# Performance work log

Measured on AMD Instinct MI355X. Metric: run time of the kernel, lower is better.

## Reference

```python
import jax, jax.numpy as jnp
import numpy as np

B, P, C, H, W = 256, 512, 512, 7, 8
T = H * W  # 56
EPS = 1e-8


def setup_inputs() -> dict:
    key = jax.random.key(0)
    k1, k2, k3 = jax.random.split(key, 3)
    inp = jax.random.normal(k1, (B, C, H, W), dtype=jnp.float32)
    # xavier-uniform-like init for prototype (fan over last two dims as torch does)
    bound_p = float(np.sqrt(6.0 / (P + C * T)))
    prototype = jax.random.uniform(k2, (P, C, T), dtype=jnp.float32, minval=-bound_p, maxval=bound_p)
    bound_w = float(np.sqrt(6.0 / (C + 1)))
    fc_w = jax.random.uniform(k3, (1, C), dtype=jnp.float32, minval=-bound_w, maxval=bound_w)
    fc_b = jnp.zeros((1,), dtype=jnp.float32)
    return {"input": inp, "prototype": prototype, "fc_w": fc_w, "fc_b": fc_b}


def reference(input, prototype, fc_w, fc_b):
    # flatten spatial dims: (B, C, T)
    x = input.reshape(input.shape[0], input.shape[1], -1)
    # per-position cosine similarity over channel dim
    dots = jnp.einsum('bct,pct->bpt', x, prototype)          # (B, P, T)
    xn = jnp.linalg.norm(x, axis=1)                           # (B, T)
    pn = jnp.linalg.norm(prototype, axis=1)                   # (P, T)
    sim = dots / jnp.maximum(xn[:, None, :] * pn[None, :, :], EPS)
    att = jax.nn.softmax(sim, axis=-1)                        # (B, P, T)
    # attention-pooled elementwise product: (B, P, C)
    feat = jnp.einsum('bpt,bct,pct->bpc', att, x, prototype)
    # fc: Linear(C, 1) then relu, view to (B, P)
    out = jax.nn.relu(jnp.einsum('bpc,oc->bpo', feat, fc_w) + fc_b)
    return out.reshape(out.shape[0], out.shape[1])
```

## Files before the change

### kernel.cpp

```cpp
#include <hip/hip_runtime.h>
#include <hip/hip_bf16.h>
#include <math.h>

constexpr int kB = 256, kC = 512, kT = 56, kP = 512;
constexpr int kCT = kC * kT;

typedef short v4s __attribute__((ext_vector_type(4)));
typedef short v8s __attribute__((ext_vector_type(8)));
typedef float v4f __attribute__((ext_vector_type(4)));
typedef float v16f __attribute__((ext_vector_type(16)));

__device__ __forceinline__ unsigned pack_bf16(float a, float b) {
  __hip_bfloat16 ha = __float2bfloat16(a);
  __hip_bfloat16 hb = __float2bfloat16(b);
  unsigned short ua, ub;
  __builtin_memcpy(&ua, &ha, 2);
  __builtin_memcpy(&ub, &hb, 2);
  return (unsigned)ua | ((unsigned)ub << 16);
}

__device__ __forceinline__ v4s frag2(unsigned w0, unsigned w1) {
  unsigned u[2] = {w0, w1};
  v4s s;
  __builtin_memcpy(&s, u, 8);
  return s;
}

__device__ __forceinline__ v8s frag8(uint4 u) {
  v8s s;
  __builtin_memcpy(&s, &u, 16);
  return s;
}

#define GLOAD(gp, lp)                                                        \
  __builtin_amdgcn_global_load_lds(                                          \
      (const __attribute__((address_space(1))) unsigned*)(const unsigned*)(gp), \
      (__attribute__((address_space(3))) unsigned*)(unsigned*)(lp), 16, 0, 0)

__global__ __launch_bounds__(512) void prep_kernel(
    const float* __restrict__ x, const float* __restrict__ proto,
    const float* __restrict__ fcw,
    unsigned* __restrict__ xt, unsigned* __restrict__ xwt,
    unsigned* __restrict__ pt,
    float* __restrict__ xn2, float* __restrict__ pn2) {
  __shared__ float tile[128 * 57];
  __shared__ float fws[512];
  __shared__ float part[8][64];

  const int tid = threadIdx.x;
  const int bidx = blockIdx.x;
  const int n = bidx >> 2;
  const int ch = bidx & 3;
  const bool isx = (n < kB);
  const int row = isx ? n : (n - kB);
  const float* src = (isx ? x : proto) + (size_t)row * kCT;

  fws[tid] = fcw[tid & 511];

  const int g = tid >> 6, tt = tid & 63;

  const float* csrc = src + ch * (128 * 56);
#pragma unroll
  for (int it = 0; it < 4; ++it) {
    const int idx = it * 512 + tid;
    if (idx < 1792) {
      const int f0 = idx * 4;
      float4 v = *(const float4*)(csrc + f0);
      int c = (int)(((unsigned)f0 * 74899u) >> 22);
      int t = f0 - c * 56;
      tile[c * 57 + t] = v.x;
      tile[c * 57 + t + 1] = v.y;
      tile[c * 57 + t + 2] = v.z;
      tile[c * 57 + t + 3] = v.w;
    }
  }
  __syncthreads();

  float nacc = 0.f;
  if (tt < 56) {
#pragma unroll
    for (int cc2 = 0; cc2 < 16; ++cc2) {
      float u = tile[(g * 16 + cc2) * 57 + tt];
      nacc = fmaf(u, u, nacc);
    }
  }

#pragma unroll
  for (int it = 0; it < 7; ++it) {
    const int id = it * 512 + tid;
    const int t = id >> 6;
    const int cw = id & 63;
    float g0 = tile[(2 * cw) * 57 + t];
    float g1 = tile[(2 * cw + 1) * 57 + t];
    unsigned wd = pack_bf16(g0, g1);
    if (isx) {
      const size_t o = ((size_t)(t * kB + row)) * 256 + ch * 64 + cw;
      const int c = ch * 128 + 2 * cw;
      xt[o] = wd;
      xwt[o] = pack_bf16(g0 * fws[c], g1 * fws[c + 1]);
    } else {
      pt[((size_t)(t * kP + row)) * 256 + ch * 64 + cw] = wd;
    }
  }

  part[g][tt] = nacc;
  __syncthreads();
  if (tid < 56) {
    float s = 0.f;
#pragma unroll
    for (int gg = 0; gg < 8; ++gg) s += part[gg][tid];
    if (isx) atomicAdd(&xn2[row * 56 + tid], s);
    else     atomicAdd(&pn2[row * 56 + tid], s);
  }
}

constexpr int TILE = 64 * 32;
constexpr int BUF = 3 * TILE;

__global__ __launch_bounds__(256, 2) void proto_gemm_kernel(
    const unsigned* __restrict__ xt, const unsigned* __restrict__ xwt,
    const unsigned* __restrict__ pt,
    const float* __restrict__ xn2, const float* __restrict__ pn2,
    float* __restrict__ part) {
  __shared__ __align__(16) unsigned lds[3 * BUF];
  __shared__ float xnL[4 * 64], pnL[4 * 64];

  const int tid = threadIdx.x;
  const int l = tid & 63;
  const int w4 = tid >> 6;
  const int wm = w4 >> 1;
  const int wn = w4 & 1;

  int bid = (int)blockIdx.x;
  bid = (bid & 7) * 56 + (bid >> 3);
  const int b0 = (bid & 3) * 64;
  const int p0 = ((bid >> 2) & 7) * 64;
  const int tg = bid >> 5;

  {
    const int tl = tid >> 6, r = tid & 63;
    xnL[tid] = sqrtf(xn2[(b0 + r) * 56 + tg * 4 + tl]);
    pnL[tid] = sqrtf(pn2[(p0 + r) * 56 + tg * 4 + tl]);
  }
  __syncthreads();

  const int lrow = l >> 3, lch = l & 7;
  size_t xsrc[2], psrc[2];
  int ldst[2];
#pragma unroll
  for (int j = 0; j < 2; ++j) {
    const int row = w4 * 16 + j * 8 + lrow;
    const int ch4 = ((lch ^ (row & 7))) * 4;
    xsrc[j] = (size_t)(b0 + row) * 256 + ch4;
    psrc[j] = (size_t)(p0 + row) * 256 + ch4;
    ldst[j] = (w4 * 16 + j * 8) * 32;
  }

  const int fr = l & 31;
  const int hi = l >> 5;
  const int axb = (wm * 32 + fr) * 32;
  const int pxb = (wn * 32 + fr) * 32;
  const int frs = fr & 7;

  v16f aD, aW, sac, nac;
#pragma unroll
  for (int i = 0; i < 16; ++i) { aD[i] = 0.f; aW[i] = 0.f; sac[i] = 0.f; nac[i] = 0.f; }

  auto STAGE = [&](int s, int buf) {
    const int t = tg * 4 + (s >> 3);
    const size_t xo = (size_t)t * (kB * 256) + (size_t)((s & 7) * 32);
    const size_t po = (size_t)t * (kP * 256) + (size_t)((s & 7) * 32);
    unsigned* lb = lds + buf * BUF;
#pragma unroll
    for (int j = 0; j < 2; ++j) {
      GLOAD(xt + xsrc[j] + xo, lb + ldst[j]);
      GLOAD(xwt + xsrc[j] + xo, lb + TILE + ldst[j]);
      GLOAD(pt + psrc[j] + po, lb + 2 * TILE + ldst[j]);
    }
  };

  auto COMPUTE = [&](int s, int buf) {
    const unsigned* bx = lds + buf * BUF;
#pragma unroll
    for (int ks = 0; ks < 4; ++ks) {
      const int col = (((ks << 1) | hi) ^ frs) << 2;
      v8s xf = frag8(*(const uint4*)(bx + axb + col));
      v8s wf = frag8(*(const uint4*)(bx + TILE + axb + col));
      v8s pf = frag8(*(const uint4*)(bx + 2 * TILE + pxb + col));
      aD = __builtin_amdgcn_mfma_f32_32x32x16_bf16(xf, pf, aD, 0, 0, 0);
      aW = __builtin_amdgcn_mfma_f32_32x32x16_bf16(wf, pf, aW, 0, 0, 0);
    }
    if ((s & 7) == 7) {
      const int tl = s >> 3;
      const float pnv = pnL[tl * 64 + wn * 32 + fr];
#pragma unroll
      for (int i = 0; i < 16; ++i) {
        const int drow = (i & 3) + 8 * (i >> 2) + 4 * hi;
        const float xnv = xnL[tl * 64 + wm * 32 + drow];
        float den = fmaxf(xnv * pnv, 1e-8f);
        float sim = aD[i] * __builtin_amdgcn_rcpf(den);
        float e = __expf(sim);
        sac[i] += e;
        nac[i] = fmaf(e, aW[i], nac[i]);
        aD[i] = 0.f;
        aW[i] = 0.f;
      }
    }
  };

  STAGE(0, 0);
  STAGE(1, 1);

  int c0 = 0, c1 = 1, c2 = 2;
#pragma unroll 1
  for (int s = 0; s < 32; ++s) {
    if (s < 31) asm volatile("s_waitcnt vmcnt(6)" ::: "memory");
    else        asm volatile("s_waitcnt vmcnt(0)" ::: "memory");
    __builtin_amdgcn_s_barrier();
    __builtin_amdgcn_sched_barrier(0);
    COMPUTE(s, c0);
    if (s < 30) STAGE(s + 2, c2);
    const int tmp = c0; c0 = c1; c1 = c2; c2 = tmp;
  }

  float* psb = part + ((size_t)tg * 2 + 0) * 131072;
  float* pnb = part + ((size_t)tg * 2 + 1) * 131072;
#pragma unroll
  for (int i = 0; i < 16; ++i) {
    const int drow = (i & 3) + 8 * (i >> 2) + 4 * hi;
    const size_t o = (size_t)(b0 + wm * 32 + drow) * 512 + p0 + wn * 32 + fr;
    psb[o] = sac[i];
    pnb[o] = nac[i];
  }
}

__global__ __launch_bounds__(256) void merge_kernel(
    const float* __restrict__ part, const float* __restrict__ fcb,
    float* __restrict__ out) {
  const int pair = blockIdx.x * 256 + threadIdx.x;
  float S = 0.f, N = 0.f;
#pragma unroll
  for (int k = 0; k < 14; ++k) {
    S += part[((size_t)k * 2 + 0) * 131072 + pair];
    N += part[((size_t)k * 2 + 1) * 131072 + pair];
  }
  float o = N * __builtin_amdgcn_rcpf(S) + fcb[0];
  out[pair] = fmaxf(o, 0.f);
}

__global__ __launch_bounds__(1024) void proto_mfma_kernel(
    const float* __restrict__ x, const float* __restrict__ proto,
    const float* __restrict__ fcw, const float* __restrict__ fcb,
    float* __restrict__ out) {
  __shared__ unsigned xs[56 * 289];
  __shared__ unsigned ps[56 * 145];
  __shared__ unsigned pws[56 * 145];

  const int tid = threadIdx.x;
  const int l = tid & 63;
  const int w = tid >> 6;
  const int bq = w & 1;
  const int tq = w >> 1;
  const int t0 = tq * 7;

  const int n = blockIdx.y * 32 + blockIdx.x;
  const int p0 = (n >> 3) * 16;
  const int b0 = (n & 7) * 32;

  const bool act = (l < 56);
  const int lt = l;

  const int xbase0 = ((b0 + 2 * w + 0) * kC) * kT + lt;
  const int xbase1 = ((b0 + 2 * w + 1) * kC) * kT + lt;
  const int pbase = ((p0 + w) * kC) * kT + lt;

  const int arow = l & 15;
  const int q2 = (l >> 4) << 1;
  const int xoff = (bq * 16 + arow) * 9 + q2;
  const int poff = arow * 9 + q2;

  v4f acc[7][2];
#pragma unroll
  for (int ti = 0; ti < 7; ++ti) {
    acc[ti][0] = v4f{0.f, 0.f, 0.f, 0.f};
    acc[ti][1] = v4f{0.f, 0.f, 0.f, 0.f};
  }
  float xn2a = 0.f, xn2b = 0.f, pn2 = 0.f;

#pragma unroll 1
  for (int st = 0; st < 32; ++st) {
    const int k0 = st * 16;
    if (act) {
#pragma unroll
      for (int r = 0; r < 16; ++r) {
        const int cw = r & 7;
        const int c = k0 + 2 * cw;
        const int ga = ((r >> 3) ? xbase1 : xbase0) + c * kT;
        float g0 = x[ga], g1 = x[ga + kT];
        if (r >> 3) xn2b = fmaf(g0, g0, fmaf(g1, g1, xn2b));
        else xn2a = fmaf(g0, g0, fmaf(g1, g1, xn2a));
        xs[lt * 289 + (2 * w + (r >> 3)) * 9 + cw] = pack_bf16(g0, g1);
      }
#pragma unroll
      for (int cw = 0; cw < 8; ++cw) {
        const int c = k0 + 2 * cw;
        const int ga = pbase + c * kT;
        float g0 = proto[ga], g1 = proto[ga + kT];
        pn2 = fmaf(g0, g0, fmaf(g1, g1, pn2));
        ps[lt * 145 + w * 9 + cw] = pack_bf16(g0, g1);
        float f0 = fcw[c], f1 = fcw[c + 1];
        pws[lt * 145 + w * 9 + cw] = pack_bf16(g0 * f0, g1 * f1);
      }
    }
    __syncthreads();
#pragma unroll
    for (int ti = 0; ti < 7; ++ti) {
      const int t = t0 + ti;
      unsigned xw0 = xs[t * 289 + xoff];
      unsigned xw1 = xs[t * 289 + xoff + 1];
      unsigned pw0 = ps[t * 145 + poff];
      unsigned pw1 = ps[t * 145 + poff + 1];
      unsigned ww0 = pws[t * 145 + poff];
      unsigned ww1 = pws[t * 145 + poff + 1];
      v4s af = frag2(xw0, xw1);
      v4s bf = frag2(pw0, pw1);
      v4s wf = frag2(ww0, ww1);
      acc[ti][0] = __builtin_amdgcn_mfma_f32_16x16x16bf16_1k(af, bf, acc[ti][0], 0, 0, 0);
      acc[ti][1] = __builtin_amdgcn_mfma_f32_16x16x16bf16_1k(af, wf, acc[ti][1], 0, 0, 0);
    }
    __syncthreads();
  }

  float* xnorm = (float*)ps;
  float* pnorm = xnorm + 32 * 56;
  if (act) {
    xnorm[(2 * w + 0) * 56 + lt] = xn2a;
    xnorm[(2 * w + 1) * 56 + lt] = xn2b;
    pnorm[w * 56 + lt] = pn2;
  }
  __syncthreads();

  float* fm = (float*)xs;
  float* fsum = fm + 4096;
  float* fnum = fsum + 4096;
  const int pc = arow;
  const int qq = l >> 4;
#pragma unroll
  for (int i = 0; i < 4; ++i) {
    const int bl = bq * 16 + 4 * qq + i;
    float m = -3.0e38f;
    float sims[7];
#pragma unroll
    for (int ti = 0; ti < 7; ++ti) {
      const int t = t0 + ti;
      float den = fmaxf(sqrtf(xnorm[bl * 56 + t]) * sqrtf(pnorm[pc * 56 + t]), 1e-8f);
      float s = acc[ti][0][i] / den;
      sims[ti] = s;
      m = fmaxf(m, s);
    }
    float se = 0.f, nu = 0.f;
#pragma unroll
    for (int ti = 0; ti < 7; ++ti) {
      float e = __expf(sims[ti] - m);
      se += e;
      nu = fmaf(e, acc[ti][1][i], nu);
    }
    const int pair = bl * 16 + pc;
    fm[tq * 512 + pair] = m;
    fsum[tq * 512 + pair] = se;
    fnum[tq * 512 + pair] = nu;
  }
  __syncthreads();

  if (tid < 512) {
    float M = -3.0e38f;
#pragma unroll
    for (int k = 0; k < 8; ++k) M = fmaxf(M, fm[k * 512 + tid]);
    float S = 0.f, N = 0.f;
#pragma unroll
    for (int k = 0; k < 8; ++k) {
      float sc = __expf(fm[k * 512 + tid] - M);
      S = fmaf(fsum[k * 512 + tid], sc, S);
      N = fmaf(fnum[k * 512 + tid], sc, N);
    }
    float o = N / S + fcb[0];
    out[(b0 + (tid >> 4)) * kP + p0 + (tid & 15)] = fmaxf(o, 0.f);
  }
}

extern "C" void kernel_launch(void* const* d_in, const int* in_sizes, int n_in,
                              void* d_out, int out_size, void* d_ws, size_t ws_size,
                              hipStream_t stream) {
  const float* x = (const float*)d_in[0];
  const float* proto = (const float*)d_in[1];
  const float* fcw = (const float*)d_in[2];
  const float* fcb = (const float*)d_in[3];
  float* out = (float*)d_out;

  const size_t need = 73572352;
  if (ws_size >= need) {
    unsigned* xt = (unsigned*)d_ws;
    unsigned* xwt = xt + 3670016;
    unsigned* ptb = xt + 7340032;
    float* partb = (float*)(xt + 14680064);
    float* xn2b = (float*)(xt + 18350080);
    float* pn2b = xn2b + 14336;

    hipMemsetAsync(xn2b, 0, (14336 + 28672) * sizeof(float), stream);

    hipLaunchKernelGGL(prep_kernel, dim3(4 * (kB + kP)), dim3(512), 0, stream,
                       x, proto, fcw, xt, xwt, ptb, xn2b, pn2b);
    hipLaunchKernelGGL(proto_gemm_kernel, dim3(448), dim3(256), 0, stream,
                       xt, xwt, ptb, xn2b, pn2b, partb);
    hipLaunchKernelGGL(merge_kernel, dim3(512), dim3(256), 0, stream,
                       partb, fcb, out);
  } else {
    hipLaunchKernelGGL(proto_mfma_kernel, dim3(32, 8), dim3(1024), 0, stream,
                       x, proto, fcw, fcb, out);
  }
}
```

Before: 67.05 us.

## Restructure prep transpose with swizzled LDS tile and vectorized bf16 stores

Rewrites the prep kernel's shared-memory transpose to use a 64-wide XOR-swizzled tile written with float4 stores. Each thread now packs eight channels per position with the hardware v_cvt_pk_bf16_f32 instruction and writes 16-byte vector stores instead of scalar 4-byte ones. The norm partials are computed from the same registers. The hipMemsetAsync is replaced with a small zeroing kernel to cut API/launch overhead. The aim is fewer LDS bank conflicts and wider global writes, at the cost of more complex indexing and an extra kernel launch.

```diff
diff --git a/kernel.cpp b/kernel.cpp
--- a/kernel.cpp
+++ b/kernel.cpp
@@ -32,10 +32,20 @@
   return s;
 }
 
+__device__ __forceinline__ unsigned cvtpk(float lo, float hi) {
+  unsigned r;
+  asm("v_cvt_pk_bf16_f32 %0, %1, %2" : "=v"(r) : "v"(lo), "v"(hi));
+  return r;
+}
+
 #define GLOAD(gp, lp)                                                        \
   __builtin_amdgcn_global_load_lds(                                          \
       (const __attribute__((address_space(1))) unsigned*)(const unsigned*)(gp), \
       (__attribute__((address_space(3))) unsigned*)(unsigned*)(lp), 16, 0, 0)
+
+__global__ __launch_bounds__(512) void zero_kernel(float* __restrict__ p) {
+  p[blockIdx.x * 512 + threadIdx.x] = 0.f;
+}
 
 __global__ __launch_bounds__(512) void prep_kernel(
     const float* __restrict__ x, const float* __restrict__ proto,
@@ -43,9 +53,8 @@
     unsigned* __restrict__ xt, unsigned* __restrict__ xwt,
     unsigned* __restrict__ pt,
     float* __restrict__ xn2, float* __restrict__ pn2) {
-  __shared__ float tile[128 * 57];
-  __shared__ float fws[512];
-  __shared__ float part[8][64];
+  __shared__ float tile[128 * 64];
+  __shared__ float normp[56 * 16];
 
   const int tid = threadIdx.x;
   const int bidx = blockIdx.x;
@@ -53,62 +62,73 @@
   const int ch = bidx & 3;
   const bool isx = (n < kB);
   const int row = isx ? n : (n - kB);
-  const float* src = (isx ? x : proto) + (size_t)row * kCT;
-
-  fws[tid] = fcw[tid & 511];
-
-  const int g = tid >> 6, tt = tid & 63;
-
-  const float* csrc = src + ch * (128 * 56);
+  const float* csrc = (isx ? x : proto) + (size_t)row * kCT + ch * (128 * 56);
+
+  const int l = tid & 63;
+  const int w = tid >> 6;
+  const int j = l & 15;
+  const int tq = l >> 4;
+
+  float fw[8];
+  if (isx) {
+    const float* gf = fcw + ch * 128 + 8 * j;
+#pragma unroll
+    for (int i = 0; i < 8; ++i) fw[i] = gf[i];
+  }
+
 #pragma unroll
   for (int it = 0; it < 4; ++it) {
     const int idx = it * 512 + tid;
     if (idx < 1792) {
       const int f0 = idx * 4;
+      const int c = (int)(((unsigned)f0 * 74899u) >> 22);
+      const int t = f0 - c * 56;
+      const int sw = ((((unsigned)c >> 3) ^ (unsigned)c) & 7) << 2;
       float4 v = *(const float4*)(csrc + f0);
-      int c = (int)(((unsigned)f0 * 74899u) >> 22);
-      int t = f0 - c * 56;
-      tile[c * 57 + t] = v.x;
-      tile[c * 57 + t + 1] = v.y;
-      tile[c * 57 + t + 2] = v.z;
-      tile[c * 57 + t + 3] = v.w;
+      *(float4*)(tile + c * 64 + (t ^ sw)) = v;
     }
   }
   __syncthreads();
 
-  float nacc = 0.f;
-  if (tt < 56) {
-#pragma unroll
-    for (int cc2 = 0; cc2 < 16; ++cc2) {
-      float u = tile[(g * 16 + cc2) * 57 + tt];
-      nacc = fmaf(u, u, nacc);
-    }
-  }
-
-#pragma unroll
-  for (int it = 0; it < 7; ++it) {
-    const int id = it * 512 + tid;
-    const int t = id >> 6;
-    const int cw = id & 63;
-    float g0 = tile[(2 * cw) * 57 + t];
-    float g1 = tile[(2 * cw + 1) * 57 + t];
-    unsigned wd = pack_bf16(g0, g1);
-    if (isx) {
-      const size_t o = ((size_t)(t * kB + row)) * 256 + ch * 64 + cw;
-      const int c = ch * 128 + 2 * cw;
-      xt[o] = wd;
-      xwt[o] = pack_bf16(g0 * fws[c], g1 * fws[c + 1]);
-    } else {
-      pt[((size_t)(t * kP + row)) * 256 + ch * 64 + cw] = wd;
-    }
-  }
-
-  part[g][tt] = nacc;
+#pragma unroll
+  for (int pass = 0; pass < 2; ++pass) {
+    const int t = pass * 32 + w * 4 + tq;
+    if (t < 56) {
+      float f[8];
+#pragma unroll
+      for (int i = 0; i < 8; ++i) {
+        const int sw = ((j ^ i) & 7) << 2;
+        f[i] = tile[(8 * j + i) * 64 + (t ^ sw)];
+      }
+      float s = 0.f;
+#pragma unroll
+      for (int i = 0; i < 8; ++i) s = fmaf(f[i], f[i], s);
+      normp[t * 16 + j] = s;
+      uint4 wx;
+      wx.x = cvtpk(f[0], f[1]);
+      wx.y = cvtpk(f[2], f[3]);
+      wx.z = cvtpk(f[4], f[5]);
+      wx.w = cvtpk(f[6], f[7]);
+      if (isx) {
+        const size_t o = ((size_t)(t * kB + row)) * 256 + ch * 64 + 4 * j;
+        *(uint4*)(xt + o) = wx;
+        uint4 ww;
+        ww.x = cvtpk(f[0] * fw[0], f[1] * fw[1]);
+        ww.y = cvtpk(f[2] * fw[2], f[3] * fw[3]);
+        ww.z = cvtpk(f[4] * fw[4], f[5] * fw[5]);
+        ww.w = cvtpk(f[6] * fw[6], f[7] * fw[7]);
+        *(uint4*)(xwt + o) = ww;
+      } else {
+        *(uint4*)(pt + ((size_t)(t * kP + row)) * 256 + ch * 64 + 4 * j) = wx;
+      }
+    }
+  }
   __syncthreads();
+
   if (tid < 56) {
     float s = 0.f;
 #pragma unroll
-    for (int gg = 0; gg < 8; ++gg) s += part[gg][tid];
+    for (int k = 0; k < 16; ++k) s += normp[tid * 16 + k];
     if (isx) atomicAdd(&xn2[row * 56 + tid], s);
     else     atomicAdd(&pn2[row * 56 + tid], s);
   }
@@ -406,7 +426,7 @@
     float* xn2b = (float*)(xt + 18350080);
     float* pn2b = xn2b + 14336;
 
-    hipMemsetAsync(xn2b, 0, (14336 + 28672) * sizeof(float), stream);
+    hipLaunchKernelGGL(zero_kernel, dim3(84), dim3(512), 0, stream, xn2b);
 
     hipLaunchKernelGGL(prep_kernel, dim3(4 * (kB + kP)), dim3(512), 0, stream,
                        x, proto, fcw, xt, xwt, ptb, xn2b, pn2b);
```

New measurement: 67.27 us. About the same (+0.3%).
